# Optimization experiments

Hardware: AMD Instinct MI355X
Metric: run time of the kernel (lower is better)

Reference implementation:

```python
import jax, jax.numpy as jnp
import numpy as np

INPUT_SIZE = 2048
HIDDEN_SIZE = 2048
BATCH = 4096
COMBINED = INPUT_SIZE + HIDDEN_SIZE


def setup_inputs() -> dict:
    key = jax.random.key(0)
    ks = jax.random.split(key, 11)
    s = 1.0 / np.sqrt(COMBINED)  # torch Linear default init scale
    inp = {
        "x_t": jax.random.normal(ks[0], (BATCH, INPUT_SIZE), jnp.float32),
        "h_prev": jax.random.normal(ks[1], (BATCH, HIDDEN_SIZE), jnp.float32),
        "c_prev": jax.random.normal(ks[2], (BATCH, HIDDEN_SIZE), jnp.float32),
        # torch nn.Linear weights: [out, in]
        "W_f": jax.random.uniform(ks[3], (HIDDEN_SIZE, COMBINED), jnp.float32, -s, s),
        "b_f": jax.random.uniform(ks[4], (HIDDEN_SIZE,), jnp.float32, -s, s),
        "W_i": jax.random.uniform(ks[5], (HIDDEN_SIZE, COMBINED), jnp.float32, -s, s),
        "b_i": jax.random.uniform(ks[6], (HIDDEN_SIZE,), jnp.float32, -s, s),
        "W_c": jax.random.uniform(ks[7], (HIDDEN_SIZE, COMBINED), jnp.float32, -s, s),
        "b_c": jax.random.uniform(ks[8], (HIDDEN_SIZE,), jnp.float32, -s, s),
        "W_o": jax.random.uniform(ks[9], (HIDDEN_SIZE, COMBINED), jnp.float32, -s, s),
        "b_o": jax.random.uniform(ks[10], (HIDDEN_SIZE,), jnp.float32, -s, s),
    }
    return inp


def reference(x_t, h_prev, c_prev, W_f, b_f, W_i, b_i, W_c, b_c, W_o, b_o):
    # combined = cat([h_prev, x_t], dim=1)  -> [B, H + I]
    combined = jnp.concatenate([h_prev, x_t], axis=1)
    # Fuse the four gate GEMMs into one [B, C] x [C, 4H] matmul.
    W = jnp.concatenate([W_f, W_i, W_c, W_o], axis=0)  # [4H, C]
    b = jnp.concatenate([b_f, b_i, b_c, b_o], axis=0)  # [4H]
    gates = combined @ W.T + b  # [B, 4H]
    gf, gi, gc, go = jnp.split(gates, 4, axis=1)
    f_t = jax.nn.sigmoid(gf)
    i_t = jax.nn.sigmoid(gi)
    c_tilde = jnp.tanh(gc)
    o_t = jax.nn.sigmoid(go)
    c_t = f_t * c_prev + i_t * c_tilde
    h_t = o_t * jnp.tanh(c_t)
    return (h_t, c_t)
```

## Files before the change

kernel.cpp:

```cpp
#include <hip/hip_runtime.h>
#include <hip/hip_bf16.h>
#include <cstdint>

#define B_DIM 4096
#define H_DIM 2048
#define I_DIM 2048
#define K_DIM 4096
#define N4    8192

typedef unsigned int u32;
typedef unsigned short u16;
typedef __attribute__((ext_vector_type(4))) float floatx4;
typedef __attribute__((ext_vector_type(8))) short bf16x8;
typedef __attribute__((ext_vector_type(8))) unsigned short ushort8_t;

__device__ static inline u16 f2bf(float f) {
    union { float f; u32 u; } v; v.f = f;
    u32 u = v.u;
    return (u16)((u + 0x7FFFu + ((u >> 16) & 1u)) >> 16);
}
__device__ static inline void gload16(const void* g, void* l) {
    __builtin_amdgcn_global_load_lds(
        (const __attribute__((address_space(1))) u32*)g,
        (__attribute__((address_space(3))) u32*)l, 16, 0, 0);
}
__device__ static inline float fast_sig(float x) {
    return 1.f / (1.f + __expf(-x));
}
__device__ static inline float fast_tanh(float x) {
    float ax = fabsf(x);
    float t = __expf(-2.f * ax);
    float r = (1.f - t) / (1.f + t);
    return copysignf(r, x);
}

__global__ void convert_all(const float* __restrict__ h_prev, const float* __restrict__ x_t,
                            const float* __restrict__ Wf, const float* __restrict__ Wi,
                            const float* __restrict__ Wc, const float* __restrict__ Wo,
                            u16* __restrict__ comb, u16* __restrict__ wb) {
    const int bid = blockIdx.x;
    const float* src;
    u16* dst;
    if (bid < 8192) {
        int base = (bid * 256 + (int)threadIdx.x) * 8;
        int row = base >> 12, col = base & 4095;
        src = (col < H_DIM) ? h_prev + (size_t)row * H_DIM + col
                            : x_t    + (size_t)row * I_DIM + (col - H_DIM);
        dst = comb + base;
    } else {
        long long base = ((long long)(bid - 8192) * 256 + threadIdx.x) * 8;
        int n = (int)(base >> 12), col = (int)(base & 4095);
        int row128 = n & 127;
        int g = (row128 >> 4) & 3;
        int j = (n >> 7) * 32 + ((row128 >> 6) << 4) + (row128 & 15);
        const float* W = (g == 0) ? Wf : (g == 1) ? Wi : (g == 2) ? Wc : Wo;
        src = W + (size_t)j * K_DIM + col;
        dst = wb + base;
    }
    float4 v0 = *(const float4*)src;
    float4 v1 = *(const float4*)(src + 4);
    ushort8_t o = { f2bf(v0.x), f2bf(v0.y), f2bf(v0.z), f2bf(v0.w),
                    f2bf(v1.x), f2bf(v1.y), f2bf(v1.z), f2bf(v1.w) };
    *(ushort8_t*)dst = o;
}

__global__ __launch_bounds__(256) void gemm_lstm(const u16* __restrict__ A,
                                                 const u16* __restrict__ Bm,
                                                 const float* __restrict__ c_prev,
                                                 const float* __restrict__ bf_,
                                                 const float* __restrict__ bi_,
                                                 const float* __restrict__ bc_,
                                                 const float* __restrict__ bo_,
                                                 float* __restrict__ out) {
    __shared__ u16 lsA[128 * 32];
    __shared__ u16 lsB[128 * 32];

    const int tid   = threadIdx.x;
    const int lane  = tid & 63;
    const int wave  = tid >> 6;
    const int wm    = (wave & 1) * 64;
    const int wpart = wave >> 1;
    const int wn    = wpart * 64;
    const int quad  = lane >> 4;
    const int r     = lane & 15;
    const int mb    = blockIdx.y * 128;
    const int nbT   = blockIdx.x * 128;

    floatx4 acc[4][4];
#pragma unroll
    for (int i = 0; i < 4; i++)
#pragma unroll
        for (int g = 0; g < 4; g++)
            acc[i][g] = (floatx4){0.f, 0.f, 0.f, 0.f};

    for (int kt = 0; kt < K_DIM; kt += 32) {
        __syncthreads();
#pragma unroll
        for (int s = 0; s < 2; s++) {
            int c   = tid + s * 256;
            int row = c >> 2;
            int ko  = (c & 3) * 8;
            gload16(A  + (size_t)(mb + row) * K_DIM + kt + ko, (char*)lsA + c * 16);
            gload16(Bm + (size_t)(nbT + row) * K_DIM + kt + ko, (char*)lsB + c * 16);
        }
        __syncthreads();

        bf16x8 af[4], bfr[4];
#pragma unroll
        for (int i = 0; i < 4; i++)
            af[i] = *(const bf16x8*)&lsA[(wm + i * 16 + r) * 32 + quad * 8];
#pragma unroll
        for (int g = 0; g < 4; g++)
            bfr[g] = *(const bf16x8*)&lsB[(wn + g * 16 + r) * 32 + quad * 8];
#pragma unroll
        for (int i = 0; i < 4; i++)
#pragma unroll
            for (int g = 0; g < 4; g++)
                acc[i][g] = __builtin_amdgcn_mfma_f32_16x16x32_bf16(
                    af[i], bfr[g], acc[i][g], 0, 0, 0);
    }

    __builtin_amdgcn_sched_barrier(0);

    const int j = blockIdx.x * 32 + wpart * 16 + r;
    const float bfv = bf_[j], biv = bi_[j], bcv = bc_[j], bov = bo_[j];
    const float* cp = c_prev + (size_t)(mb + wm + quad * 4) * H_DIM + j;
    float* oh = out + (size_t)(mb + wm + quad * 4) * H_DIM + j;
    float* oc = oh + (size_t)B_DIM * H_DIM;
#pragma unroll
    for (int i = 0; i < 4; i++) {
#pragma unroll
        for (int rg = 0; rg < 4; rg++) {
            size_t off = (size_t)(i * 16 + rg) * H_DIM;
            float gf = acc[i][0][rg] + bfv;
            float gi = acc[i][1][rg] + biv;
            float gc = acc[i][2][rg] + bcv;
            float go = acc[i][3][rg] + bov;
            float f  = fast_sig(gf);
            float ii = fast_sig(gi);
            float ct = fast_tanh(gc);
            float oo = fast_sig(go);
            float c = f * cp[off] + ii * ct;
            float h = oo * fast_tanh(c);
            oh[off] = h;
            oc[off] = c;
        }
    }
}

__global__ void lstm_naive(const float* __restrict__ x_t, const float* __restrict__ h_prev,
                           const float* __restrict__ c_prev,
                           const float* __restrict__ Wf, const float* __restrict__ bf_,
                           const float* __restrict__ Wi, const float* __restrict__ bi_,
                           const float* __restrict__ Wc, const float* __restrict__ bc_,
                           const float* __restrict__ Wo, const float* __restrict__ bo_,
                           float* __restrict__ out) {
    int j = blockIdx.x * blockDim.x + threadIdx.x;
    int b = blockIdx.y;
    const float* hrow = h_prev + (long long)b * H_DIM;
    const float* xrow = x_t   + (long long)b * I_DIM;
    const float* wf = Wf + (long long)j * K_DIM;
    const float* wi = Wi + (long long)j * K_DIM;
    const float* wc = Wc + (long long)j * K_DIM;
    const float* wo = Wo + (long long)j * K_DIM;
    float af = bf_[j], ai = bi_[j], ac = bc_[j], ao = bo_[j];
    for (int k = 0; k < H_DIM; k += 4) {
        float4 v = *(const float4*)(hrow + k);
        float4 a = *(const float4*)(wf + k);
        float4 bqi = *(const float4*)(wi + k);
        float4 cq = *(const float4*)(wc + k);
        float4 dq = *(const float4*)(wo + k);
        af += v.x*a.x + v.y*a.y + v.z*a.z + v.w*a.w;
        ai += v.x*bqi.x + v.y*bqi.y + v.z*bqi.z + v.w*bqi.w;
        ac += v.x*cq.x + v.y*cq.y + v.z*cq.z + v.w*cq.w;
        ao += v.x*dq.x + v.y*dq.y + v.z*dq.z + v.w*dq.w;
    }
    for (int k = 0; k < I_DIM; k += 4) {
        float4 v = *(const float4*)(xrow + k);
        float4 a = *(const float4*)(wf + H_DIM + k);
        float4 bqi = *(const float4*)(wi + H_DIM + k);
        float4 cq = *(const float4*)(wc + H_DIM + k);
        float4 dq = *(const float4*)(wo + H_DIM + k);
        af += v.x*a.x + v.y*a.y + v.z*a.z + v.w*a.w;
        ai += v.x*bqi.x + v.y*bqi.y + v.z*bqi.z + v.w*bqi.w;
        ac += v.x*cq.x + v.y*cq.y + v.z*cq.z + v.w*cq.w;
        ao += v.x*dq.x + v.y*dq.y + v.z*dq.z + v.w*dq.w;
    }
    float f  = 1.f / (1.f + __expf(-af));
    float ii = 1.f / (1.f + __expf(-ai));
    float ct = tanhf(ac);
    float oo = 1.f / (1.f + __expf(-ao));
    int t = b * H_DIM + j;
    float c = f * c_prev[t] + ii * ct;
    out[t] = oo * tanhf(c);
    out[B_DIM * H_DIM + t] = c;
}

extern "C" void kernel_launch(void* const* d_in, const int* in_sizes, int n_in,
                              void* d_out, int out_size, void* d_ws, size_t ws_size,
                              hipStream_t stream) {
    const float* x_t    = (const float*)d_in[0];
    const float* h_prev = (const float*)d_in[1];
    const float* c_prev = (const float*)d_in[2];
    const float* Wf = (const float*)d_in[3];  const float* bf_ = (const float*)d_in[4];
    const float* Wi = (const float*)d_in[5];  const float* bi_ = (const float*)d_in[6];
    const float* Wc = (const float*)d_in[7];  const float* bc_ = (const float*)d_in[8];
    const float* Wo = (const float*)d_in[9];  const float* bo_ = (const float*)d_in[10];
    float* out = (float*)d_out;

    const size_t comb_elems = (size_t)B_DIM * K_DIM;
    const size_t wb_elems   = (size_t)N4 * K_DIM;
    const size_t need = (comb_elems + wb_elems) * sizeof(u16);

    if (ws_size >= need) {
        u16* comb = (u16*)d_ws;
        u16* wb   = comb + comb_elems;
        convert_all<<<24576, 256, 0, stream>>>(h_prev, x_t, Wf, Wi, Wc, Wo, comb, wb);
        dim3 grid(N4 / 128, B_DIM / 128);
        gemm_lstm<<<grid, 256, 0, stream>>>(comb, wb, c_prev, bf_, bi_, bc_, bo_, out);
    } else {
        dim3 grid(H_DIM / 256, B_DIM);
        lstm_naive<<<grid, 256, 0, stream>>>(x_t, h_prev, c_prev,
                                             Wf, bf_, Wi, bi_, Wc, bc_, Wo, bo_, out);
    }
}
```

Measured before the change: 568.7 us.

## Use 256x256 GEMM tiles with 4-stage LDS pipeline and swizzled shared memory

Rewrites the fused LSTM gate GEMM to use 512-thread blocks with 256x256 output tiles and a four-buffer LDS ring. Global-to-LDS loads run three K-steps ahead, with manual vmcnt waits and a single barrier per step. This replaces the previous two-barrier load-then-compute loop. LDS chunk offsets are XOR-swizzled to cut bank conflicts, MFMA sections get raised wave priority, and the bf16 conversion uses a vector convert builtin. The trade-offs are about 128KB of LDS per block, which limits each CU to one block, and higher register pressure from 32 accumulators per lane.

```diff
diff --git a/kernel.cpp b/kernel.cpp
--- a/kernel.cpp
+++ b/kernel.cpp
@@ -12,13 +12,9 @@
 typedef unsigned short u16;
 typedef __attribute__((ext_vector_type(4))) float floatx4;
 typedef __attribute__((ext_vector_type(8))) short bf16x8;
-typedef __attribute__((ext_vector_type(8))) unsigned short ushort8_t;
-
-__device__ static inline u16 f2bf(float f) {
-    union { float f; u32 u; } v; v.f = f;
-    u32 u = v.u;
-    return (u16)((u + 0x7FFFu + ((u >> 16) & 1u)) >> 16);
-}
+typedef __attribute__((ext_vector_type(8))) float f32x8;
+typedef __attribute__((ext_vector_type(8))) __bf16 bfx8;
+
 __device__ static inline void gload16(const void* g, void* l) {
     __builtin_amdgcn_global_load_lds(
         (const __attribute__((address_space(1))) u32*)g,
@@ -59,78 +55,100 @@
     }
     float4 v0 = *(const float4*)src;
     float4 v1 = *(const float4*)(src + 4);
-    ushort8_t o = { f2bf(v0.x), f2bf(v0.y), f2bf(v0.z), f2bf(v0.w),
-                    f2bf(v1.x), f2bf(v1.y), f2bf(v1.z), f2bf(v1.w) };
-    *(ushort8_t*)dst = o;
-}
-
-__global__ __launch_bounds__(256) void gemm_lstm(const u16* __restrict__ A,
-                                                 const u16* __restrict__ Bm,
-                                                 const float* __restrict__ c_prev,
-                                                 const float* __restrict__ bf_,
-                                                 const float* __restrict__ bi_,
-                                                 const float* __restrict__ bc_,
-                                                 const float* __restrict__ bo_,
-                                                 float* __restrict__ out) {
-    __shared__ u16 lsA[128 * 32];
-    __shared__ u16 lsB[128 * 32];
-
-    const int tid   = threadIdx.x;
-    const int lane  = tid & 63;
-    const int wave  = tid >> 6;
-    const int wm    = (wave & 1) * 64;
-    const int wpart = wave >> 1;
-    const int wn    = wpart * 64;
-    const int quad  = lane >> 4;
-    const int r     = lane & 15;
-    const int mb    = blockIdx.y * 128;
-    const int nbT   = blockIdx.x * 128;
-
-    floatx4 acc[4][4];
-#pragma unroll
-    for (int i = 0; i < 4; i++)
-#pragma unroll
-        for (int g = 0; g < 4; g++)
+    f32x8 f = { v0.x, v0.y, v0.z, v0.w, v1.x, v1.y, v1.z, v1.w };
+    *(bfx8*)dst = __builtin_convertvector(f, bfx8);
+}
+
+__device__ static inline void stage32(const u16* __restrict__ A, const u16* __restrict__ Bm,
+                                      u16* dA, u16* dB, int mb, int nbT, int kt, int tid) {
+#pragma unroll
+    for (int s = 0; s < 2; ++s) {
+        int c = tid + s * 512;
+        int row = c >> 2;
+        int ko = ((c & 3) ^ ((c >> 3) & 3)) * 8;
+        gload16(A + (size_t)(mb + row) * K_DIM + kt + ko, (char*)dA + c * 16);
+        gload16(Bm + (size_t)(nbT + row) * K_DIM + kt + ko, (char*)dB + c * 16);
+    }
+}
+
+__global__ __launch_bounds__(512, 2) void gemm_lstm(const u16* __restrict__ A,
+                                                    const u16* __restrict__ Bm,
+                                                    const float* __restrict__ c_prev,
+                                                    const float* __restrict__ bf_,
+                                                    const float* __restrict__ bi_,
+                                                    const float* __restrict__ bc_,
+                                                    const float* __restrict__ bo_,
+                                                    float* __restrict__ out) {
+    __shared__ __align__(16) u16 lsA[4][256 * 32];
+    __shared__ __align__(16) u16 lsB[4][256 * 32];
+
+    const int tid  = threadIdx.x;
+    const int lane = tid & 63;
+    const int wave = tid >> 6;
+    const int wm2  = (wave >> 2) * 128;
+    const int wn2  = (wave & 3) * 64;
+    const int quad = lane >> 4;
+    const int r    = lane & 15;
+    const int qsw  = (quad ^ ((r >> 1) & 3)) * 8;
+    const int mb   = blockIdx.y * 256;
+    const int nbT  = blockIdx.x * 256;
+
+    floatx4 acc[8][4];
+#pragma unroll
+    for (int i = 0; i < 8; ++i)
+#pragma unroll
+        for (int g = 0; g < 4; ++g)
             acc[i][g] = (floatx4){0.f, 0.f, 0.f, 0.f};
 
-    for (int kt = 0; kt < K_DIM; kt += 32) {
-        __syncthreads();
-#pragma unroll
-        for (int s = 0; s < 2; s++) {
-            int c   = tid + s * 256;
-            int row = c >> 2;
-            int ko  = (c & 3) * 8;
-            gload16(A  + (size_t)(mb + row) * K_DIM + kt + ko, (char*)lsA + c * 16);
-            gload16(Bm + (size_t)(nbT + row) * K_DIM + kt + ko, (char*)lsB + c * 16);
+#pragma unroll
+    for (int pt = 0; pt < 3; ++pt)
+        stage32(A, Bm, lsA[pt], lsB[pt], mb, nbT, pt * 32, tid);
+
+#pragma unroll 4
+    for (int t = 0; t < 128; ++t) {
+        if (t < 126) {
+            asm volatile("s_waitcnt vmcnt(8)" ::: "memory");
+        } else {
+            asm volatile("s_waitcnt vmcnt(0)" ::: "memory");
         }
-        __syncthreads();
-
-        bf16x8 af[4], bfr[4];
-#pragma unroll
-        for (int i = 0; i < 4; i++)
-            af[i] = *(const bf16x8*)&lsA[(wm + i * 16 + r) * 32 + quad * 8];
-#pragma unroll
-        for (int g = 0; g < 4; g++)
-            bfr[g] = *(const bf16x8*)&lsB[(wn + g * 16 + r) * 32 + quad * 8];
-#pragma unroll
-        for (int i = 0; i < 4; i++)
-#pragma unroll
-            for (int g = 0; g < 4; g++)
+        __builtin_amdgcn_s_barrier();
+        __builtin_amdgcn_sched_barrier(0);
+
+        if (t < 125)
+            stage32(A, Bm, lsA[(t + 3) & 3], lsB[(t + 3) & 3], mb, nbT, (t + 3) * 32, tid);
+
+        const u16* sA = lsA[t & 3];
+        const u16* sB = lsB[t & 3];
+        bf16x8 af[8], bb[4];
+#pragma unroll
+        for (int i = 0; i < 8; ++i)
+            af[i] = *(const bf16x8*)&sA[(wm2 + i * 16 + r) * 32 + qsw];
+#pragma unroll
+        for (int g = 0; g < 4; ++g)
+            bb[g] = *(const bf16x8*)&sB[(wn2 + g * 16 + r) * 32 + qsw];
+
+        __builtin_amdgcn_s_setprio(1);
+#pragma unroll
+        for (int i = 0; i < 8; ++i)
+#pragma unroll
+            for (int g = 0; g < 4; ++g)
                 acc[i][g] = __builtin_amdgcn_mfma_f32_16x16x32_bf16(
-                    af[i], bfr[g], acc[i][g], 0, 0, 0);
+                    af[i], bb[g], acc[i][g], 0, 0, 0);
+        __builtin_amdgcn_s_setprio(0);
     }
 
     __builtin_amdgcn_sched_barrier(0);
 
-    const int j = blockIdx.x * 32 + wpart * 16 + r;
+    const int j = blockIdx.x * 64 + (wave & 3) * 16 + r;
     const float bfv = bf_[j], biv = bi_[j], bcv = bc_[j], bov = bo_[j];
-    const float* cp = c_prev + (size_t)(mb + wm + quad * 4) * H_DIM + j;
-    float* oh = out + (size_t)(mb + wm + quad * 4) * H_DIM + j;
+    const int rowb = mb + wm2 + quad * 4;
+    const float* cp = c_prev + (size_t)rowb * H_DIM + j;
+    float* oh = out + (size_t)rowb * H_DIM + j;
     float* oc = oh + (size_t)B_DIM * H_DIM;
 #pragma unroll
-    for (int i = 0; i < 4; i++) {
-#pragma unroll
-        for (int rg = 0; rg < 4; rg++) {
+    for (int i = 0; i < 8; ++i) {
+#pragma unroll
+        for (int rg = 0; rg < 4; ++rg) {
             size_t off = (size_t)(i * 16 + rg) * H_DIM;
             float gf = acc[i][0][rg] + bfv;
             float gi = acc[i][1][rg] + biv;
@@ -140,8 +158,8 @@
             float ii = fast_sig(gi);
             float ct = fast_tanh(gc);
             float oo = fast_sig(go);
-            float c = f * cp[off] + ii * ct;
-            float h = oo * fast_tanh(c);
+            float c  = f * cp[off] + ii * ct;
+            float h  = oo * fast_tanh(c);
             oh[off] = h;
             oc[off] = c;
         }
@@ -216,8 +234,8 @@
         u16* comb = (u16*)d_ws;
         u16* wb   = comb + comb_elems;
         convert_all<<<24576, 256, 0, stream>>>(h_prev, x_t, Wf, Wi, Wc, Wo, comb, wb);
-        dim3 grid(N4 / 128, B_DIM / 128);
-        gemm_lstm<<<grid, 256, 0, stream>>>(comb, wb, c_prev, bf_, bi_, bc_, bo_, out);
+        dim3 grid(N4 / 256, B_DIM / 256);
+        gemm_lstm<<<grid, 512, 0, stream>>>(comb, wb, c_prev, bf_, bi_, bc_, bo_, out);
     } else {
         dim3 grid(H_DIM / 256, B_DIM);
         lstm_naive<<<grid, 256, 0, stream>>>(x_t, h_prev, c_prev,
```

Result: faster. 489.8 us (-13.9%).
